# Performance work log

Measured on AMD Instinct MI355X. Metric: run time of the kernel, lower is better.

The kernel has to match this reference:

```python
import jax, jax.numpy as jnp
import numpy as np

HEADS = 4
DIM_HEAD = 32
EPS = 1e-5


def setup_inputs() -> dict:
    key = jax.random.key(0)
    ks = jax.random.split(key, 3)
    B, H, W, C = 16, 64, 64, 128
    hidden = HEADS * DIM_HEAD  # 128
    x = jax.random.normal(ks[0], (B, H, W, C), dtype=jnp.float32)
    w_qkv = jax.random.normal(ks[1], (C, 3 * hidden), dtype=jnp.float32) * 0.05
    w_out = jax.random.normal(ks[2], (hidden, C), dtype=jnp.float32) * 0.05
    b_out = jnp.zeros((C,), dtype=jnp.float32)
    g_ln = jnp.ones((C,), dtype=jnp.float32)
    b_ln = jnp.zeros((C,), dtype=jnp.float32)
    return {"x": x, "w_qkv": w_qkv, "w_out": w_out, "b_out": b_out,
            "g_ln": g_ln, "b_ln": b_ln}


def reference(x, w_qkv, w_out, b_out, g_ln, b_ln):
    B, H, W, C = x.shape
    scale = DIM_HEAD ** -0.5
    n = H * W
    # 1x1 conv == channel matmul: [B,H,W,C] @ [C,3*hidden]
    qkv = jnp.einsum('bhwc,cf->bhwf', x, w_qkv)
    q, k, v = jnp.split(qkv, 3, axis=-1)
    # rearrange 'b x y (h c) -> b h c (x y)'
    def to_heads(t):
        return t.reshape(B, n, HEADS, DIM_HEAD).transpose(0, 2, 3, 1)  # [B,h,d,n]
    q, k, v = map(to_heads, (q, k, v))
    q = jax.nn.softmax(q, axis=-2) * scale   # softmax over channel dim d
    k = jax.nn.softmax(k, axis=-1)           # softmax over spatial dim n
    context = jnp.einsum('bhdn,bhen->bhde', k, v)  # [B,h,d,e] small
    out = jnp.einsum('bhde,bhdn->bhen', context, q)  # [B,h,e,n]
    # rearrange 'b h c (x y) -> b x y (h c)'
    out = out.transpose(0, 3, 1, 2).reshape(B, H, W, HEADS * DIM_HEAD)
    # to_out: 1x1 conv with bias, then LayerNorm over last dim
    out = jnp.einsum('bhwc,cd->bhwd', out, w_out) + b_out
    mean = jnp.mean(out, axis=-1, keepdims=True)
    var = jnp.var(out, axis=-1, keepdims=True)
    out = (out - mean) / jnp.sqrt(var + EPS) * g_ln + b_ln
    return out
```

## Files before the change

kernel.cpp:

```cpp
#include <hip/hip_runtime.h>
#include <hip/hip_bf16.h>
#include <cstddef>
#include <cstdint>


typedef __attribute__((ext_vector_type(8))) short short8_t;
typedef __attribute__((ext_vector_type(4))) float f32x4;

#define SCALE_Q 0.17677669529663687f
#define EPS_LN 1e-5f

__device__ __forceinline__ unsigned short f2bf(float f) {
  union { float f; unsigned u; } v; v.f = f;
  unsigned r = (v.u + 0x7FFFu + ((v.u >> 16) & 1u)) >> 16;
  return (unsigned short)r;
}
__device__ __forceinline__ float bf2f(unsigned short u) {
  union { float f; unsigned u; } v; v.u = ((unsigned)u) << 16;
  return v.f;
}

__device__ __forceinline__ short8_t trunc8(float4 lo, float4 hi) {
  union { float4 f; unsigned u[4]; } a, b;
  union { unsigned u[4]; short8_t s; } r;
  a.f = lo; b.f = hi;
  r.u[0] = __builtin_amdgcn_perm(a.u[1], a.u[0], 0x07060302);
  r.u[1] = __builtin_amdgcn_perm(a.u[3], a.u[2], 0x07060302);
  r.u[2] = __builtin_amdgcn_perm(b.u[1], b.u[0], 0x07060302);
  r.u[3] = __builtin_amdgcn_perm(b.u[3], b.u[2], 0x07060302);
  return r.s;
}

__global__ void k_transpose_wqkv(const float* __restrict__ w,
                                 unsigned short* __restrict__ wT) {
  int idx = blockIdx.x * 256 + threadIdx.x;
  int k = idx / 384;
  int c = idx - k * 384;
  wT[c * 128 + k] = f2bf(w[idx]);
}

__global__ __launch_bounds__(256, 2)
void k_qkv_ctx(const float* __restrict__ x, const unsigned short* __restrict__ wT,
               float* __restrict__ ctxp, float* __restrict__ ksump,
               unsigned short* __restrict__ qs) {
  __shared__ short ekT[128][136];
  __shared__ short vT[128][136];

  int tid = threadIdx.x;
  int rb = blockIdx.x;
  int rowBase = rb * 128;

  int lane = tid & 63;
  int wv = tid >> 6;
  int wr = wv >> 1, wc = wv & 1;
  int lr = lane & 15;
  int kg = lane >> 4;

  short8_t abf[4][4];
  {
    const float* ap = x + (size_t)(rowBase + wr * 64 + lr) * 128 + kg * 8;
#pragma unroll
    for (int mf = 0; mf < 4; ++mf) {
      const float* r = ap + (size_t)mf * 16 * 128;
#pragma unroll
      for (int kk = 0; kk < 4; ++kk)
        abf[kk][mf] = trunc8(*(const float4*)(r + kk * 32),
                             *(const float4*)(r + kk * 32 + 4));
    }
  }

  const unsigned short* wq = wT;
  const unsigned short* wk = wT + 16384;
  const unsigned short* wvv = wT + 32768;
  int bRow[4];
#pragma unroll
  for (int nf = 0; nf < 4; ++nf) bRow[nf] = (wc * 64 + nf * 16 + lr) * 128;

  {
    f32x4 acc[4][4] = {};
#pragma unroll
    for (int kk = 0; kk < 4; ++kk) {
      short8_t bf[4];
#pragma unroll
      for (int nf = 0; nf < 4; ++nf)
        bf[nf] = *(const short8_t*)(wk + bRow[nf] + kk * 32 + kg * 8);
#pragma unroll
      for (int mf = 0; mf < 4; ++mf)
#pragma unroll
        for (int nf = 0; nf < 4; ++nf)
          acc[mf][nf] = __builtin_amdgcn_mfma_f32_16x16x32_bf16(abf[kk][mf], bf[nf], acc[mf][nf], 0, 0, 0);
    }
#pragma unroll
    for (int mf = 0; mf < 4; ++mf) {
      int t0 = wr * 64 + mf * 16 + kg * 4;
#pragma unroll
      for (int nf = 0; nf < 4; ++nf) {
        unsigned s0 = f2bf(__expf(acc[mf][nf][0])), s1 = f2bf(__expf(acc[mf][nf][1]));
        unsigned s2 = f2bf(__expf(acc[mf][nf][2])), s3 = f2bf(__expf(acc[mf][nf][3]));
        uint2 p; p.x = s0 | (s1 << 16); p.y = s2 | (s3 << 16);
        *(uint2*)&ekT[wc * 64 + nf * 16 + lr][t0] = p;
      }
    }
  }
  {
    f32x4 acc[4][4] = {};
#pragma unroll
    for (int kk = 0; kk < 4; ++kk) {
      short8_t bf[4];
#pragma unroll
      for (int nf = 0; nf < 4; ++nf)
        bf[nf] = *(const short8_t*)(wvv + bRow[nf] + kk * 32 + kg * 8);
#pragma unroll
      for (int mf = 0; mf < 4; ++mf)
#pragma unroll
        for (int nf = 0; nf < 4; ++nf)
          acc[mf][nf] = __builtin_amdgcn_mfma_f32_16x16x32_bf16(abf[kk][mf], bf[nf], acc[mf][nf], 0, 0, 0);
    }
#pragma unroll
    for (int mf = 0; mf < 4; ++mf) {
      int t0 = wr * 64 + mf * 16 + kg * 4;
#pragma unroll
      for (int nf = 0; nf < 4; ++nf) {
        unsigned s0 = f2bf(acc[mf][nf][0]), s1 = f2bf(acc[mf][nf][1]);
        unsigned s2 = f2bf(acc[mf][nf][2]), s3 = f2bf(acc[mf][nf][3]);
        uint2 p; p.x = s0 | (s1 << 16); p.y = s2 | (s3 << 16);
        *(uint2*)&vT[wc * 64 + nf * 16 + lr][t0] = p;
      }
    }
  }

  f32x4 qacc[4][4] = {};
#pragma unroll
  for (int kk = 0; kk < 4; ++kk) {
    short8_t bf[4];
#pragma unroll
    for (int nf = 0; nf < 4; ++nf)
      bf[nf] = *(const short8_t*)(wq + bRow[nf] + kk * 32 + kg * 8);
#pragma unroll
    for (int mf = 0; mf < 4; ++mf)
#pragma unroll
      for (int nf = 0; nf < 4; ++nf)
        qacc[mf][nf] = __builtin_amdgcn_mfma_f32_16x16x32_bf16(abf[kk][mf], bf[nf], qacc[mf][nf], 0, 0, 0);
  }

  __syncthreads();

  {
    int h = wv;
    f32x4 c2[2][2] = {};
#pragma unroll
    for (int kk = 0; kk < 4; ++kk) {
      short8_t a2[2], b2[2];
#pragma unroll
      for (int m2 = 0; m2 < 2; ++m2)
        a2[m2] = *(const short8_t*)&ekT[h * 32 + m2 * 16 + lr][kk * 32 + kg * 8];
#pragma unroll
      for (int n2 = 0; n2 < 2; ++n2)
        b2[n2] = *(const short8_t*)&vT[h * 32 + n2 * 16 + lr][kk * 32 + kg * 8];
#pragma unroll
      for (int m2 = 0; m2 < 2; ++m2)
#pragma unroll
        for (int n2 = 0; n2 < 2; ++n2)
          c2[m2][n2] = __builtin_amdgcn_mfma_f32_16x16x32_bf16(a2[m2], b2[n2], c2[m2][n2], 0, 0, 0);
    }
    float* cp = ctxp + ((size_t)rb * 4 + h) * 1024;
#pragma unroll
    for (int m2 = 0; m2 < 2; ++m2)
#pragma unroll
      for (int n2 = 0; n2 < 2; ++n2)
#pragma unroll
        for (int j = 0; j < 4; ++j)
          cp[(m2 * 16 + kg * 4 + j) * 32 + n2 * 16 + lr] = c2[m2][n2][j];
  }

  if (tid < 128) {
    float s = 0;
#pragma unroll
    for (int t8 = 0; t8 < 128; t8 += 8) {
      short8_t v8 = *(const short8_t*)&ekT[tid][t8];
#pragma unroll
      for (int i = 0; i < 8; ++i) s += bf2f((unsigned short)v8[i]);
    }
    ksump[(size_t)rb * 128 + tid] = s;
  }

#pragma unroll
  for (int hg = 0; hg < 2; ++hg) {
#pragma unroll
    for (int mf = 0; mf < 4; ++mf) {
#pragma unroll
      for (int j = 0; j < 4; ++j) {
        float e0 = __expf(qacc[mf][hg * 2][j]);
        float e1 = __expf(qacc[mf][hg * 2 + 1][j]);
        float s = e0 + e1;
#pragma unroll
        for (int d = 1; d < 16; d <<= 1) s += __shfl_xor(s, d, 64);
        float inv = SCALE_Q / s;
        int tok = rowBase + wr * 64 + mf * 16 + kg * 4 + j;
        int hd = wc * 64 + hg * 32 + lr;
        qs[(size_t)tok * 128 + hd] = f2bf(e0 * inv);
        qs[(size_t)tok * 128 + hd + 16] = f2bf(e1 * inv);
      }
    }
  }
}

__global__ __launch_bounds__(256, 4)
void k_weff64(const float* __restrict__ ctxp, const float* __restrict__ ksump,
              const float* __restrict__ wout, unsigned short* __restrict__ weffT) {
  __shared__ float wo[32][128];
  __shared__ float cn[32][32];
  __shared__ float ksh[32];
  int tid = threadIdx.x;
  int b = blockIdx.x >> 2, h = blockIdx.x & 3;

#pragma unroll
  for (int i = 0; i < 16; ++i) {
    int idx = i * 256 + tid;
    int e = idx >> 7, jj = idx & 127;
    wo[e][jj] = wout[(h * 32 + e) * 128 + jj];
  }
  if (tid < 32) {
    float s = 0;
    for (int c = 0; c < 32; ++c)
      s += ksump[(size_t)(b * 32 + c) * 128 + h * 32 + tid];
    ksh[tid] = s;
  }
  __syncthreads();
#pragma unroll
  for (int i = 0; i < 4; ++i) {
    int idx = i * 256 + tid;
    int d = idx >> 5, e = idx & 31;
    float s = 0;
    for (int c = 0; c < 32; ++c)
      s += ctxp[((size_t)(b * 32 + c) * 4 + h) * 1024 + idx];
    cn[d][e] = s / ksh[d];
  }
  __syncthreads();

  int j = tid >> 1, dg = tid & 1;
  unsigned short acc16[16];
#pragma unroll
  for (int dd = 0; dd < 16; ++dd) {
    int d = dg * 16 + dd;
    float s = 0;
#pragma unroll
    for (int e = 0; e < 32; ++e) s += cn[d][e] * wo[e][j];
    acc16[dd] = f2bf(s);
  }
  unsigned short* outp = weffT + (size_t)b * 16384 + j * 128 + h * 32 + dg * 16;
  *(short8_t*)outp = *(short8_t*)&acc16[0];
  *(short8_t*)(outp + 8) = *(short8_t*)&acc16[8];
}

__global__ __launch_bounds__(256, 2)
void k_out_ln(const unsigned short* __restrict__ qs, const unsigned short* __restrict__ weffT,
              const float* __restrict__ b_out, const float* __restrict__ g_ln,
              const float* __restrict__ b_ln, float* __restrict__ out) {
  int tid = threadIdx.x;
  int rowBase = blockIdx.x * 128;
  int b = rowBase >> 12;
  int lane = tid & 63;
  int w = tid >> 6;
  int lr = lane & 15;
  int kg = lane >> 4;

  const unsigned short* bb = weffT + (size_t)b * 16384;

  short8_t a[2][4];
  {
    const unsigned short* ap = qs + (size_t)(rowBase + w * 32 + lr) * 128 + kg * 8;
#pragma unroll
    for (int mf = 0; mf < 2; ++mf)
#pragma unroll
      for (int kk = 0; kk < 4; ++kk)
        a[mf][kk] = *(const short8_t*)(ap + (size_t)mf * 16 * 128 + kk * 32);
  }

  f32x4 acc[2][8] = {};
#pragma unroll
  for (int kk = 0; kk < 4; ++kk) {
    short8_t bf[8];
#pragma unroll
    for (int nf = 0; nf < 8; ++nf)
      bf[nf] = *(const short8_t*)(bb + (size_t)(nf * 16 + lr) * 128 + kk * 32 + kg * 8);
#pragma unroll
    for (int mf = 0; mf < 2; ++mf)
#pragma unroll
      for (int nf = 0; nf < 8; ++nf)
        acc[mf][nf] = __builtin_amdgcn_mfma_f32_16x16x32_bf16(a[mf][kk], bf[nf], acc[mf][nf], 0, 0, 0);
  }

  float bo[8], gl[8], bl[8];
#pragma unroll
  for (int nf = 0; nf < 8; ++nf) {
    int c = nf * 16 + lr;
    bo[nf] = b_out[c]; gl[nf] = g_ln[c]; bl[nf] = b_ln[c];
  }
#pragma unroll
  for (int mf = 0; mf < 2; ++mf)
#pragma unroll
    for (int nf = 0; nf < 8; ++nf)
#pragma unroll
      for (int j = 0; j < 4; ++j) acc[mf][nf][j] += bo[nf];

#pragma unroll
  for (int mf = 0; mf < 2; ++mf) {
    float s[4] = {0, 0, 0, 0}, q[4] = {0, 0, 0, 0};
#pragma unroll
    for (int nf = 0; nf < 8; ++nf)
#pragma unroll
      for (int j = 0; j < 4; ++j) {
        float v = acc[mf][nf][j];
        s[j] += v; q[j] += v * v;
      }
#pragma unroll
    for (int j = 0; j < 4; ++j) {
#pragma unroll
      for (int d = 1; d < 16; d <<= 1) {
        s[j] += __shfl_xor(s[j], d, 64);
        q[j] += __shfl_xor(q[j], d, 64);
      }
    }
#pragma unroll
    for (int j = 0; j < 4; ++j) {
      float mean = s[j] * (1.0f / 128.0f);
      float var = q[j] * (1.0f / 128.0f) - mean * mean;
      float rstd = rsqrtf(var + EPS_LN);
      size_t ro = (size_t)(rowBase + w * 32 + mf * 16 + kg * 4 + j) * 128;
#pragma unroll
      for (int nf = 0; nf < 8; ++nf)
        out[ro + nf * 16 + lr] = (acc[mf][nf][j] - mean) * rstd * gl[nf] + bl[nf];
    }
  }
}

extern "C" void kernel_launch(void* const* d_in, const int* in_sizes, int n_in,
                              void* d_out, int out_size, void* d_ws, size_t ws_size,
                              hipStream_t stream) {
  const float* x     = (const float*)d_in[0];
  const float* w_qkv = (const float*)d_in[1];
  const float* w_out = (const float*)d_in[2];
  const float* b_out = (const float*)d_in[3];
  const float* g_ln  = (const float*)d_in[4];
  const float* b_ln  = (const float*)d_in[5];
  float* out = (float*)d_out;

  char* ws = (char*)d_ws;
  unsigned short* wqkvT = (unsigned short*)(ws + 0);
  float* ctxp           = (float*)(ws + 131072);
  float* ksump          = (float*)(ws + 131072 + 8388608);
  unsigned short* weffT = (unsigned short*)(ws + 131072 + 8388608 + 262144);
  unsigned short* qs    = (unsigned short*)(ws + 131072 + 8388608 + 262144 + 524288);

  k_transpose_wqkv<<<192, 256, 0, stream>>>(w_qkv, wqkvT);
  k_qkv_ctx<<<512, 256, 0, stream>>>(x, wqkvT, ctxp, ksump, qs);
  k_weff64<<<64, 256, 0, stream>>>(ctxp, ksump, w_out, weffT);
  k_out_ln<<<512, 256, 0, stream>>>(qs, weffT, b_out, g_ln, b_ln, out);
}
```

Before: 62.16 us.

## Split fused QKV kernel into Q-softmax and KV-context kernels with LDS-staged weights

Splits the combined QKV projection/context kernel into two: one computes Q projection plus channel softmax on 64-row tiles, the other computes K/V projections and the per-block context. Both stage their weight slices in shared memory instead of reading from global per wave, and the weight transpose now writes packed pairs. The aim is lower register pressure and better occupancy than the old kernel, which held Q accumulators live across K/V work. In exchange, x is read twice from global memory and there is an extra kernel launch.

```diff
diff --git a/kernel.cpp b/kernel.cpp
--- a/kernel.cpp
+++ b/kernel.cpp
@@ -33,22 +33,30 @@
 
 __global__ void k_transpose_wqkv(const float* __restrict__ w,
                                  unsigned short* __restrict__ wT) {
-  int idx = blockIdx.x * 256 + threadIdx.x;
-  int k = idx / 384;
-  int c = idx - k * 384;
-  wT[c * 128 + k] = f2bf(w[idx]);
-}
-
-__global__ __launch_bounds__(256, 2)
-void k_qkv_ctx(const float* __restrict__ x, const unsigned short* __restrict__ wT,
-               float* __restrict__ ctxp, float* __restrict__ ksump,
-               unsigned short* __restrict__ qs) {
-  __shared__ short ekT[128][136];
-  __shared__ short vT[128][136];
-
+  int c = blockIdx.x * 4 + (threadIdx.x >> 6);
+  int l = threadIdx.x & 63;
+  float f0 = w[(size_t)(2 * l) * 384 + c];
+  float f1 = w[(size_t)(2 * l + 1) * 384 + c];
+  unsigned p = (unsigned)f2bf(f0) | ((unsigned)f2bf(f1) << 16);
+  ((unsigned*)(wT + (size_t)c * 128))[l] = p;
+}
+
+__global__ __launch_bounds__(256, 4)
+void k_q_soft(const float* __restrict__ x, const unsigned short* __restrict__ wT,
+              unsigned short* __restrict__ qs) {
+  __shared__ short Bq[128][136];
   int tid = threadIdx.x;
-  int rb = blockIdx.x;
-  int rowBase = rb * 128;
+  int rowBase = blockIdx.x * 64;
+
+  {
+#pragma unroll
+    for (int i = 0; i < 8; ++i) {
+      int idx = i * 256 + tid;
+      int n = idx >> 4;
+      int k8 = (idx & 15) << 3;
+      *(short8_t*)&Bq[n][k8] = *(const short8_t*)(wT + (size_t)n * 128 + k8);
+    }
+  }
 
   int lane = tid & 63;
   int wv = tid >> 6;
@@ -56,11 +64,11 @@
   int lr = lane & 15;
   int kg = lane >> 4;
 
-  short8_t abf[4][4];
-  {
-    const float* ap = x + (size_t)(rowBase + wr * 64 + lr) * 128 + kg * 8;
-#pragma unroll
-    for (int mf = 0; mf < 4; ++mf) {
+  short8_t abf[4][2];
+  {
+    const float* ap = x + (size_t)(rowBase + wr * 32 + lr) * 128 + kg * 8;
+#pragma unroll
+    for (int mf = 0; mf < 2; ++mf) {
       const float* r = ap + (size_t)mf * 16 * 128;
 #pragma unroll
       for (int kk = 0; kk < 4; ++kk)
@@ -68,140 +76,188 @@
                              *(const float4*)(r + kk * 32 + 4));
     }
   }
-
-  const unsigned short* wq = wT;
-  const unsigned short* wk = wT + 16384;
-  const unsigned short* wvv = wT + 32768;
-  int bRow[4];
-#pragma unroll
-  for (int nf = 0; nf < 4; ++nf) bRow[nf] = (wc * 64 + nf * 16 + lr) * 128;
-
-  {
-    f32x4 acc[4][4] = {};
-#pragma unroll
-    for (int kk = 0; kk < 4; ++kk) {
-      short8_t bf[4];
-#pragma unroll
-      for (int nf = 0; nf < 4; ++nf)
-        bf[nf] = *(const short8_t*)(wk + bRow[nf] + kk * 32 + kg * 8);
-#pragma unroll
-      for (int mf = 0; mf < 4; ++mf)
-#pragma unroll
-        for (int nf = 0; nf < 4; ++nf)
-          acc[mf][nf] = __builtin_amdgcn_mfma_f32_16x16x32_bf16(abf[kk][mf], bf[nf], acc[mf][nf], 0, 0, 0);
-    }
-#pragma unroll
-    for (int mf = 0; mf < 4; ++mf) {
-      int t0 = wr * 64 + mf * 16 + kg * 4;
-#pragma unroll
-      for (int nf = 0; nf < 4; ++nf) {
-        unsigned s0 = f2bf(__expf(acc[mf][nf][0])), s1 = f2bf(__expf(acc[mf][nf][1]));
-        unsigned s2 = f2bf(__expf(acc[mf][nf][2])), s3 = f2bf(__expf(acc[mf][nf][3]));
-        uint2 p; p.x = s0 | (s1 << 16); p.y = s2 | (s3 << 16);
-        *(uint2*)&ekT[wc * 64 + nf * 16 + lr][t0] = p;
-      }
-    }
-  }
-  {
-    f32x4 acc[4][4] = {};
-#pragma unroll
-    for (int kk = 0; kk < 4; ++kk) {
-      short8_t bf[4];
-#pragma unroll
-      for (int nf = 0; nf < 4; ++nf)
-        bf[nf] = *(const short8_t*)(wvv + bRow[nf] + kk * 32 + kg * 8);
-#pragma unroll
-      for (int mf = 0; mf < 4; ++mf)
-#pragma unroll
-        for (int nf = 0; nf < 4; ++nf)
-          acc[mf][nf] = __builtin_amdgcn_mfma_f32_16x16x32_bf16(abf[kk][mf], bf[nf], acc[mf][nf], 0, 0, 0);
-    }
-#pragma unroll
-    for (int mf = 0; mf < 4; ++mf) {
-      int t0 = wr * 64 + mf * 16 + kg * 4;
-#pragma unroll
-      for (int nf = 0; nf < 4; ++nf) {
-        unsigned s0 = f2bf(acc[mf][nf][0]), s1 = f2bf(acc[mf][nf][1]);
-        unsigned s2 = f2bf(acc[mf][nf][2]), s3 = f2bf(acc[mf][nf][3]);
-        uint2 p; p.x = s0 | (s1 << 16); p.y = s2 | (s3 << 16);
-        *(uint2*)&vT[wc * 64 + nf * 16 + lr][t0] = p;
-      }
-    }
-  }
-
-  f32x4 qacc[4][4] = {};
+  __syncthreads();
+
+  f32x4 acc[2][4] = {};
 #pragma unroll
   for (int kk = 0; kk < 4; ++kk) {
     short8_t bf[4];
 #pragma unroll
     for (int nf = 0; nf < 4; ++nf)
-      bf[nf] = *(const short8_t*)(wq + bRow[nf] + kk * 32 + kg * 8);
-#pragma unroll
-    for (int mf = 0; mf < 4; ++mf)
+      bf[nf] = *(const short8_t*)&Bq[wc * 64 + nf * 16 + lr][kk * 32 + kg * 8];
+#pragma unroll
+    for (int mf = 0; mf < 2; ++mf)
 #pragma unroll
       for (int nf = 0; nf < 4; ++nf)
-        qacc[mf][nf] = __builtin_amdgcn_mfma_f32_16x16x32_bf16(abf[kk][mf], bf[nf], qacc[mf][nf], 0, 0, 0);
-  }
-
-  __syncthreads();
-
-  {
-    int h = wv;
-    f32x4 c2[2][2] = {};
-#pragma unroll
-    for (int kk = 0; kk < 4; ++kk) {
-      short8_t a2[2], b2[2];
-#pragma unroll
-      for (int m2 = 0; m2 < 2; ++m2)
-        a2[m2] = *(const short8_t*)&ekT[h * 32 + m2 * 16 + lr][kk * 32 + kg * 8];
-#pragma unroll
-      for (int n2 = 0; n2 < 2; ++n2)
-        b2[n2] = *(const short8_t*)&vT[h * 32 + n2 * 16 + lr][kk * 32 + kg * 8];
-#pragma unroll
-      for (int m2 = 0; m2 < 2; ++m2)
-#pragma unroll
-        for (int n2 = 0; n2 < 2; ++n2)
-          c2[m2][n2] = __builtin_amdgcn_mfma_f32_16x16x32_bf16(a2[m2], b2[n2], c2[m2][n2], 0, 0, 0);
-    }
-    float* cp = ctxp + ((size_t)rb * 4 + h) * 1024;
-#pragma unroll
-    for (int m2 = 0; m2 < 2; ++m2)
-#pragma unroll
-      for (int n2 = 0; n2 < 2; ++n2)
-#pragma unroll
-        for (int j = 0; j < 4; ++j)
-          cp[(m2 * 16 + kg * 4 + j) * 32 + n2 * 16 + lr] = c2[m2][n2][j];
-  }
-
-  if (tid < 128) {
-    float s = 0;
-#pragma unroll
-    for (int t8 = 0; t8 < 128; t8 += 8) {
-      short8_t v8 = *(const short8_t*)&ekT[tid][t8];
-#pragma unroll
-      for (int i = 0; i < 8; ++i) s += bf2f((unsigned short)v8[i]);
-    }
-    ksump[(size_t)rb * 128 + tid] = s;
+        acc[mf][nf] = __builtin_amdgcn_mfma_f32_16x16x32_bf16(abf[kk][mf], bf[nf], acc[mf][nf], 0, 0, 0);
   }
 
 #pragma unroll
   for (int hg = 0; hg < 2; ++hg) {
 #pragma unroll
-    for (int mf = 0; mf < 4; ++mf) {
+    for (int mf = 0; mf < 2; ++mf) {
 #pragma unroll
       for (int j = 0; j < 4; ++j) {
-        float e0 = __expf(qacc[mf][hg * 2][j]);
-        float e1 = __expf(qacc[mf][hg * 2 + 1][j]);
+        float e0 = __expf(acc[mf][hg * 2][j]);
+        float e1 = __expf(acc[mf][hg * 2 + 1][j]);
         float s = e0 + e1;
 #pragma unroll
         for (int d = 1; d < 16; d <<= 1) s += __shfl_xor(s, d, 64);
         float inv = SCALE_Q / s;
-        int tok = rowBase + wr * 64 + mf * 16 + kg * 4 + j;
+        int tok = rowBase + wr * 32 + mf * 16 + kg * 4 + j;
         int hd = wc * 64 + hg * 32 + lr;
         qs[(size_t)tok * 128 + hd] = f2bf(e0 * inv);
         qs[(size_t)tok * 128 + hd + 16] = f2bf(e1 * inv);
       }
     }
+  }
+}
+
+__global__ __launch_bounds__(256, 2)
+void k_kv_ctx(const float* __restrict__ x, const unsigned short* __restrict__ wT,
+              float* __restrict__ ctxp, float* __restrict__ ksump) {
+  __shared__ short Bk[128][136];
+  __shared__ short Bv[128][136];
+
+  int tid = threadIdx.x;
+  int rb = blockIdx.x;
+  int rowBase = rb * 128;
+
+  {
+    const unsigned short* wk = wT + (size_t)1 * 128 * 128;
+    const unsigned short* wv2 = wT + (size_t)2 * 128 * 128;
+#pragma unroll
+    for (int i = 0; i < 8; ++i) {
+      int idx = i * 256 + tid;
+      int n = idx >> 4;
+      int k8 = (idx & 15) << 3;
+      *(short8_t*)&Bk[n][k8] = *(const short8_t*)(wk + (size_t)n * 128 + k8);
+      *(short8_t*)&Bv[n][k8] = *(const short8_t*)(wv2 + (size_t)n * 128 + k8);
+    }
+  }
+
+  int lane = tid & 63;
+  int wv = tid >> 6;
+  int wr = wv >> 1, wc = wv & 1;
+  int lr = lane & 15;
+  int kg = lane >> 4;
+
+  short8_t abf[4][4];
+  {
+    const float* ap = x + (size_t)(rowBase + wr * 64 + lr) * 128 + kg * 8;
+#pragma unroll
+    for (int mf = 0; mf < 4; ++mf) {
+      const float* r = ap + (size_t)mf * 16 * 128;
+#pragma unroll
+      for (int kk = 0; kk < 4; ++kk)
+        abf[kk][mf] = trunc8(*(const float4*)(r + kk * 32),
+                             *(const float4*)(r + kk * 32 + 4));
+    }
+  }
+  __syncthreads();
+
+  uint2 ekp[4][4], vp[4][4];
+  {
+    f32x4 acc[4][4] = {};
+#pragma unroll
+    for (int kk = 0; kk < 4; ++kk) {
+      short8_t bf[4];
+#pragma unroll
+      for (int nf = 0; nf < 4; ++nf)
+        bf[nf] = *(const short8_t*)&Bk[wc * 64 + nf * 16 + lr][kk * 32 + kg * 8];
+#pragma unroll
+      for (int mf = 0; mf < 4; ++mf)
+#pragma unroll
+        for (int nf = 0; nf < 4; ++nf)
+          acc[mf][nf] = __builtin_amdgcn_mfma_f32_16x16x32_bf16(abf[kk][mf], bf[nf], acc[mf][nf], 0, 0, 0);
+    }
+#pragma unroll
+    for (int mf = 0; mf < 4; ++mf)
+#pragma unroll
+      for (int nf = 0; nf < 4; ++nf) {
+        unsigned s0 = f2bf(__expf(acc[mf][nf][0])), s1 = f2bf(__expf(acc[mf][nf][1]));
+        unsigned s2 = f2bf(__expf(acc[mf][nf][2])), s3 = f2bf(__expf(acc[mf][nf][3]));
+        ekp[mf][nf].x = s0 | (s1 << 16);
+        ekp[mf][nf].y = s2 | (s3 << 16);
+      }
+  }
+  {
+    f32x4 acc[4][4] = {};
+#pragma unroll
+    for (int kk = 0; kk < 4; ++kk) {
+      short8_t bf[4];
+#pragma unroll
+      for (int nf = 0; nf < 4; ++nf)
+        bf[nf] = *(const short8_t*)&Bv[wc * 64 + nf * 16 + lr][kk * 32 + kg * 8];
+#pragma unroll
+      for (int mf = 0; mf < 4; ++mf)
+#pragma unroll
+        for (int nf = 0; nf < 4; ++nf)
+          acc[mf][nf] = __builtin_amdgcn_mfma_f32_16x16x32_bf16(abf[kk][mf], bf[nf], acc[mf][nf], 0, 0, 0);
+    }
+#pragma unroll
+    for (int mf = 0; mf < 4; ++mf)
+#pragma unroll
+      for (int nf = 0; nf < 4; ++nf) {
+        unsigned s0 = f2bf(acc[mf][nf][0]), s1 = f2bf(acc[mf][nf][1]);
+        unsigned s2 = f2bf(acc[mf][nf][2]), s3 = f2bf(acc[mf][nf][3]);
+        vp[mf][nf].x = s0 | (s1 << 16);
+        vp[mf][nf].y = s2 | (s3 << 16);
+      }
+  }
+  __syncthreads();
+
+  short (*ekT)[136] = Bk;
+  short (*vT)[136] = Bv;
+#pragma unroll
+  for (int mf = 0; mf < 4; ++mf) {
+    int t0 = wr * 64 + mf * 16 + kg * 4;
+#pragma unroll
+    for (int nf = 0; nf < 4; ++nf) {
+      int col = wc * 64 + nf * 16 + lr;
+      *(uint2*)&ekT[col][t0] = ekp[mf][nf];
+      *(uint2*)&vT[col][t0] = vp[mf][nf];
+    }
+  }
+  __syncthreads();
+
+  {
+    int h = wv;
+    f32x4 c2[2][2] = {};
+#pragma unroll
+    for (int kk = 0; kk < 4; ++kk) {
+      short8_t a2[2], b2[2];
+#pragma unroll
+      for (int m2 = 0; m2 < 2; ++m2)
+        a2[m2] = *(const short8_t*)&ekT[h * 32 + m2 * 16 + lr][kk * 32 + kg * 8];
+#pragma unroll
+      for (int n2 = 0; n2 < 2; ++n2)
+        b2[n2] = *(const short8_t*)&vT[h * 32 + n2 * 16 + lr][kk * 32 + kg * 8];
+#pragma unroll
+      for (int m2 = 0; m2 < 2; ++m2)
+#pragma unroll
+        for (int n2 = 0; n2 < 2; ++n2)
+          c2[m2][n2] = __builtin_amdgcn_mfma_f32_16x16x32_bf16(a2[m2], b2[n2], c2[m2][n2], 0, 0, 0);
+    }
+    float* cp = ctxp + ((size_t)rb * 4 + h) * 1024;
+#pragma unroll
+    for (int m2 = 0; m2 < 2; ++m2)
+#pragma unroll
+      for (int n2 = 0; n2 < 2; ++n2)
+#pragma unroll
+        for (int j = 0; j < 4; ++j)
+          cp[(m2 * 16 + kg * 4 + j) * 32 + n2 * 16 + lr] = c2[m2][n2][j];
+  }
+
+  if (tid < 128) {
+    float s = 0;
+#pragma unroll
+    for (int t8 = 0; t8 < 128; t8 += 8) {
+      short8_t v8 = *(const short8_t*)&ekT[tid][t8];
+#pragma unroll
+      for (int i = 0; i < 8; ++i) s += bf2f((unsigned short)v8[i]);
+    }
+    ksump[(size_t)rb * 128 + tid] = s;
   }
 }
 
@@ -353,8 +409,9 @@
   unsigned short* weffT = (unsigned short*)(ws + 131072 + 8388608 + 262144);
   unsigned short* qs    = (unsigned short*)(ws + 131072 + 8388608 + 262144 + 524288);
 
-  k_transpose_wqkv<<<192, 256, 0, stream>>>(w_qkv, wqkvT);
-  k_qkv_ctx<<<512, 256, 0, stream>>>(x, wqkvT, ctxp, ksump, qs);
+  k_transpose_wqkv<<<96, 256, 0, stream>>>(w_qkv, wqkvT);
+  k_q_soft<<<1024, 256, 0, stream>>>(x, wqkvT, qs);
+  k_kv_ctx<<<512, 256, 0, stream>>>(x, wqkvT, ctxp, ksump);
   k_weff64<<<64, 256, 0, stream>>>(ctxp, ksump, w_out, weffT);
   k_out_ln<<<512, 256, 0, stream>>>(qs, weffT, b_out, g_ln, b_ln, out);
 }
```

Measured after the change: 63.07 us. About the same (+1.5%).

## Restructure QKV kernel: batch loads, MFMA key sums, early Q softmax

Applied to the files above, without the earlier changes.

The QKV/context kernel now issues all x loads and all weight fragments for each GEMM up front. It holds the exp(K) and V results in registers and writes them to LDS together. The Q softmax and its store are moved before the barrier so they overlap other waves' work, and the per-row key sums are computed with an extra MFMA against a ones vector instead of a scalar loop. The weight transpose kernel is rewritten so each thread handles a column pair with packed stores, and the LDS row padding changes from 136 to 132. Register pressure rises from the prefetched fragments and held packed results, and the new padding may change bank conflicts.

```diff
diff --git a/kernel.cpp b/kernel.cpp
--- a/kernel.cpp
+++ b/kernel.cpp
@@ -33,23 +33,24 @@
 
 __global__ void k_transpose_wqkv(const float* __restrict__ w,
                                  unsigned short* __restrict__ wT) {
-  int idx = blockIdx.x * 256 + threadIdx.x;
-  int k = idx / 384;
-  int c = idx - k * 384;
-  wT[c * 128 + k] = f2bf(w[idx]);
+  int c = blockIdx.x * 4 + (threadIdx.x >> 6);
+  int l = threadIdx.x & 63;
+  float f0 = w[(size_t)(2 * l) * 384 + c];
+  float f1 = w[(size_t)(2 * l + 1) * 384 + c];
+  unsigned p = (unsigned)f2bf(f0) | ((unsigned)f2bf(f1) << 16);
+  ((unsigned*)(wT + (size_t)c * 128))[l] = p;
 }
 
 __global__ __launch_bounds__(256, 2)
-void k_qkv_ctx(const float* __restrict__ x, const unsigned short* __restrict__ wT,
-               float* __restrict__ ctxp, float* __restrict__ ksump,
-               unsigned short* __restrict__ qs) {
-  __shared__ short ekT[128][136];
-  __shared__ short vT[128][136];
+void k_qkv_mega(const float* __restrict__ x, const unsigned short* __restrict__ wT,
+                float* __restrict__ ctxp, float* __restrict__ ksump,
+                unsigned short* __restrict__ qs) {
+  __shared__ short ekT[128][132];
+  __shared__ short vT[128][132];
 
   int tid = threadIdx.x;
   int rb = blockIdx.x;
   int rowBase = rb * 128;
-
   int lane = tid & 63;
   int wv = tid >> 6;
   int wr = wv >> 1, wc = wv & 1;
@@ -60,12 +61,22 @@
   {
     const float* ap = x + (size_t)(rowBase + wr * 64 + lr) * 128 + kg * 8;
 #pragma unroll
-    for (int mf = 0; mf < 4; ++mf) {
-      const float* r = ap + (size_t)mf * 16 * 128;
-#pragma unroll
-      for (int kk = 0; kk < 4; ++kk)
-        abf[kk][mf] = trunc8(*(const float4*)(r + kk * 32),
-                             *(const float4*)(r + kk * 32 + 4));
+    for (int half = 0; half < 2; ++half) {
+      float4 xr[16];
+#pragma unroll
+      for (int mh = 0; mh < 2; ++mh) {
+        const float* r = ap + (size_t)(half * 2 + mh) * 16 * 128;
+#pragma unroll
+        for (int kk = 0; kk < 4; ++kk) {
+          xr[mh * 8 + kk * 2]     = *(const float4*)(r + kk * 32);
+          xr[mh * 8 + kk * 2 + 1] = *(const float4*)(r + kk * 32 + 4);
+        }
+      }
+#pragma unroll
+      for (int mh = 0; mh < 2; ++mh)
+#pragma unroll
+        for (int kk = 0; kk < 4; ++kk)
+          abf[kk][half * 2 + mh] = trunc8(xr[mh * 8 + kk * 2], xr[mh * 8 + kk * 2 + 1]);
     }
   }
 
@@ -76,78 +87,117 @@
 #pragma unroll
   for (int nf = 0; nf < 4; ++nf) bRow[nf] = (wc * 64 + nf * 16 + lr) * 128;
 
-  {
+  uint2 ekp[4][4], vp[4][4];
+
+  {
+    short8_t bfr[4][4];
+#pragma unroll
+    for (int kk = 0; kk < 4; ++kk)
+#pragma unroll
+      for (int nf = 0; nf < 4; ++nf)
+        bfr[kk][nf] = *(const short8_t*)(wk + bRow[nf] + kk * 32 + kg * 8);
     f32x4 acc[4][4] = {};
 #pragma unroll
-    for (int kk = 0; kk < 4; ++kk) {
-      short8_t bf[4];
-#pragma unroll
-      for (int nf = 0; nf < 4; ++nf)
-        bf[nf] = *(const short8_t*)(wk + bRow[nf] + kk * 32 + kg * 8);
+    for (int kk = 0; kk < 4; ++kk)
 #pragma unroll
       for (int mf = 0; mf < 4; ++mf)
 #pragma unroll
         for (int nf = 0; nf < 4; ++nf)
-          acc[mf][nf] = __builtin_amdgcn_mfma_f32_16x16x32_bf16(abf[kk][mf], bf[nf], acc[mf][nf], 0, 0, 0);
-    }
-#pragma unroll
-    for (int mf = 0; mf < 4; ++mf) {
-      int t0 = wr * 64 + mf * 16 + kg * 4;
+          acc[mf][nf] = __builtin_amdgcn_mfma_f32_16x16x32_bf16(abf[kk][mf], bfr[kk][nf], acc[mf][nf], 0, 0, 0);
+#pragma unroll
+    for (int mf = 0; mf < 4; ++mf)
 #pragma unroll
       for (int nf = 0; nf < 4; ++nf) {
         unsigned s0 = f2bf(__expf(acc[mf][nf][0])), s1 = f2bf(__expf(acc[mf][nf][1]));
         unsigned s2 = f2bf(__expf(acc[mf][nf][2])), s3 = f2bf(__expf(acc[mf][nf][3]));
-        uint2 p; p.x = s0 | (s1 << 16); p.y = s2 | (s3 << 16);
-        *(uint2*)&ekT[wc * 64 + nf * 16 + lr][t0] = p;
-      }
-    }
-  }
-  {
+        ekp[mf][nf].x = s0 | (s1 << 16);
+        ekp[mf][nf].y = s2 | (s3 << 16);
+      }
+  }
+  {
+    short8_t bfr[4][4];
+#pragma unroll
+    for (int kk = 0; kk < 4; ++kk)
+#pragma unroll
+      for (int nf = 0; nf < 4; ++nf)
+        bfr[kk][nf] = *(const short8_t*)(wvv + bRow[nf] + kk * 32 + kg * 8);
     f32x4 acc[4][4] = {};
 #pragma unroll
-    for (int kk = 0; kk < 4; ++kk) {
-      short8_t bf[4];
-#pragma unroll
-      for (int nf = 0; nf < 4; ++nf)
-        bf[nf] = *(const short8_t*)(wvv + bRow[nf] + kk * 32 + kg * 8);
+    for (int kk = 0; kk < 4; ++kk)
 #pragma unroll
       for (int mf = 0; mf < 4; ++mf)
 #pragma unroll
         for (int nf = 0; nf < 4; ++nf)
-          acc[mf][nf] = __builtin_amdgcn_mfma_f32_16x16x32_bf16(abf[kk][mf], bf[nf], acc[mf][nf], 0, 0, 0);
-    }
-#pragma unroll
-    for (int mf = 0; mf < 4; ++mf) {
-      int t0 = wr * 64 + mf * 16 + kg * 4;
+          acc[mf][nf] = __builtin_amdgcn_mfma_f32_16x16x32_bf16(abf[kk][mf], bfr[kk][nf], acc[mf][nf], 0, 0, 0);
+#pragma unroll
+    for (int mf = 0; mf < 4; ++mf)
 #pragma unroll
       for (int nf = 0; nf < 4; ++nf) {
         unsigned s0 = f2bf(acc[mf][nf][0]), s1 = f2bf(acc[mf][nf][1]);
         unsigned s2 = f2bf(acc[mf][nf][2]), s3 = f2bf(acc[mf][nf][3]);
-        uint2 p; p.x = s0 | (s1 << 16); p.y = s2 | (s3 << 16);
-        *(uint2*)&vT[wc * 64 + nf * 16 + lr][t0] = p;
-      }
-    }
-  }
-
-  f32x4 qacc[4][4] = {};
-#pragma unroll
-  for (int kk = 0; kk < 4; ++kk) {
-    short8_t bf[4];
-#pragma unroll
-    for (int nf = 0; nf < 4; ++nf)
-      bf[nf] = *(const short8_t*)(wq + bRow[nf] + kk * 32 + kg * 8);
-#pragma unroll
-    for (int mf = 0; mf < 4; ++mf)
+        vp[mf][nf].x = s0 | (s1 << 16);
+        vp[mf][nf].y = s2 | (s3 << 16);
+      }
+  }
+
+#pragma unroll
+  for (int mf = 0; mf < 4; ++mf) {
+    int t0 = wr * 64 + mf * 16 + kg * 4;
+#pragma unroll
+    for (int nf = 0; nf < 4; ++nf) {
+      int col = wc * 64 + nf * 16 + lr;
+      *(uint2*)&ekT[col][t0] = ekp[mf][nf];
+      *(uint2*)&vT[col][t0] = vp[mf][nf];
+    }
+  }
+
+  {
+    short8_t bfr[4][4];
+#pragma unroll
+    for (int kk = 0; kk < 4; ++kk)
 #pragma unroll
       for (int nf = 0; nf < 4; ++nf)
-        qacc[mf][nf] = __builtin_amdgcn_mfma_f32_16x16x32_bf16(abf[kk][mf], bf[nf], qacc[mf][nf], 0, 0, 0);
+        bfr[kk][nf] = *(const short8_t*)(wq + bRow[nf] + kk * 32 + kg * 8);
+    f32x4 qacc[4][4] = {};
+#pragma unroll
+    for (int kk = 0; kk < 4; ++kk)
+#pragma unroll
+      for (int mf = 0; mf < 4; ++mf)
+#pragma unroll
+        for (int nf = 0; nf < 4; ++nf)
+          qacc[mf][nf] = __builtin_amdgcn_mfma_f32_16x16x32_bf16(abf[kk][mf], bfr[kk][nf], qacc[mf][nf], 0, 0, 0);
+
+#pragma unroll
+    for (int hg = 0; hg < 2; ++hg) {
+#pragma unroll
+      for (int mf = 0; mf < 4; ++mf) {
+#pragma unroll
+        for (int j = 0; j < 4; ++j) {
+          float e0 = __expf(qacc[mf][hg * 2][j]);
+          float e1 = __expf(qacc[mf][hg * 2 + 1][j]);
+          float s = e0 + e1;
+#pragma unroll
+          for (int d = 1; d < 16; d <<= 1) s += __shfl_xor(s, d, 64);
+          float inv = SCALE_Q / s;
+          int tok = rowBase + wr * 64 + mf * 16 + kg * 4 + j;
+          int hd = wc * 64 + hg * 32 + lr;
+          qs[(size_t)tok * 128 + hd] = f2bf(e0 * inv);
+          qs[(size_t)tok * 128 + hd + 16] = f2bf(e1 * inv);
+        }
+      }
+    }
   }
 
   __syncthreads();
 
   {
     int h = wv;
+    union { unsigned u[4]; short8_t s; } ones;
+#pragma unroll
+    for (int i = 0; i < 4; ++i) ones.u[i] = 0x3F803F80u;
+
     f32x4 c2[2][2] = {};
+    f32x4 ks2[2] = {};
 #pragma unroll
     for (int kk = 0; kk < 4; ++kk) {
       short8_t a2[2], b2[2];
@@ -158,10 +208,12 @@
       for (int n2 = 0; n2 < 2; ++n2)
         b2[n2] = *(const short8_t*)&vT[h * 32 + n2 * 16 + lr][kk * 32 + kg * 8];
 #pragma unroll
-      for (int m2 = 0; m2 < 2; ++m2)
+      for (int m2 = 0; m2 < 2; ++m2) {
 #pragma unroll
         for (int n2 = 0; n2 < 2; ++n2)
           c2[m2][n2] = __builtin_amdgcn_mfma_f32_16x16x32_bf16(a2[m2], b2[n2], c2[m2][n2], 0, 0, 0);
+        ks2[m2] = __builtin_amdgcn_mfma_f32_16x16x32_bf16(a2[m2], ones.s, ks2[m2], 0, 0, 0);
+      }
     }
     float* cp = ctxp + ((size_t)rb * 4 + h) * 1024;
 #pragma unroll
@@ -171,36 +223,12 @@
 #pragma unroll
         for (int j = 0; j < 4; ++j)
           cp[(m2 * 16 + kg * 4 + j) * 32 + n2 * 16 + lr] = c2[m2][n2][j];
-  }
-
-  if (tid < 128) {
-    float s = 0;
-#pragma unroll
-    for (int t8 = 0; t8 < 128; t8 += 8) {
-      short8_t v8 = *(const short8_t*)&ekT[tid][t8];
-#pragma unroll
-      for (int i = 0; i < 8; ++i) s += bf2f((unsigned short)v8[i]);
-    }
-    ksump[(size_t)rb * 128 + tid] = s;
-  }
-
-#pragma unroll
-  for (int hg = 0; hg < 2; ++hg) {
-#pragma unroll
-    for (int mf = 0; mf < 4; ++mf) {
-#pragma unroll
-      for (int j = 0; j < 4; ++j) {
-        float e0 = __expf(qacc[mf][hg * 2][j]);
-        float e1 = __expf(qacc[mf][hg * 2 + 1][j]);
-        float s = e0 + e1;
-#pragma unroll
-        for (int d = 1; d < 16; d <<= 1) s += __shfl_xor(s, d, 64);
-        float inv = SCALE_Q / s;
-        int tok = rowBase + wr * 64 + mf * 16 + kg * 4 + j;
-        int hd = wc * 64 + hg * 32 + lr;
-        qs[(size_t)tok * 128 + hd] = f2bf(e0 * inv);
-        qs[(size_t)tok * 128 + hd + 16] = f2bf(e1 * inv);
-      }
+    if (lr == 0) {
+#pragma unroll
+      for (int m2 = 0; m2 < 2; ++m2)
+#pragma unroll
+        for (int j = 0; j < 4; ++j)
+          ksump[(size_t)rb * 128 + h * 32 + m2 * 16 + kg * 4 + j] = ks2[m2][j];
     }
   }
 }
@@ -230,11 +258,11 @@
 #pragma unroll
   for (int i = 0; i < 4; ++i) {
     int idx = i * 256 + tid;
-    int d = idx >> 5, e = idx & 31;
+    int d = idx >> 5;
     float s = 0;
     for (int c = 0; c < 32; ++c)
       s += ctxp[((size_t)(b * 32 + c) * 4 + h) * 1024 + idx];
-    cn[d][e] = s / ksh[d];
+    cn[d][idx & 31] = s / ksh[d];
   }
   __syncthreads();
 
@@ -353,8 +381,8 @@
   unsigned short* weffT = (unsigned short*)(ws + 131072 + 8388608 + 262144);
   unsigned short* qs    = (unsigned short*)(ws + 131072 + 8388608 + 262144 + 524288);
 
-  k_transpose_wqkv<<<192, 256, 0, stream>>>(w_qkv, wqkvT);
-  k_qkv_ctx<<<512, 256, 0, stream>>>(x, wqkvT, ctxp, ksump, qs);
+  k_transpose_wqkv<<<96, 256, 0, stream>>>(w_qkv, wqkvT);
+  k_qkv_mega<<<512, 256, 0, stream>>>(x, wqkvT, ctxp, ksump, qs);
   k_weff64<<<64, 256, 0, stream>>>(ctxp, ksump, w_out, weffT);
   k_out_ln<<<512, 256, 0, stream>>>(qs, weffT, b_out, g_ln, b_ln, out);
 }
```

Result: no change. 61.50 us (-1.1%).
